# Kernel optimization log

Measured on AMD Instinct MI355X. Metric: run time of the kernel, lower is better.

Reference implementation:

```python
import jax, jax.numpy as jnp
import numpy as np

HIDDEN = 2048
N_HEADS = 32
N_KV_HEADS = 4
HEAD_DIM = 128
EPS = 1e-6
ROPE_THETA = 1000000.0
B, S = 1, 2048


def setup_inputs() -> dict:
    key = jax.random.key(0)
    ks = jax.random.split(key, 7)
    scale = 0.02
    return {
        "hidden_states": jax.random.normal(ks[0], (B, S, HIDDEN), jnp.float32),
        "wq": jax.random.normal(ks[1], (HIDDEN, N_HEADS * HEAD_DIM), jnp.float32) * scale,
        "wk": jax.random.normal(ks[2], (HIDDEN, N_KV_HEADS * HEAD_DIM), jnp.float32) * scale,
        "wv": jax.random.normal(ks[3], (HIDDEN, N_KV_HEADS * HEAD_DIM), jnp.float32) * scale,
        "wo": jax.random.normal(ks[4], (N_HEADS * HEAD_DIM, HIDDEN), jnp.float32) * scale,
        "q_norm_w": jnp.ones((HEAD_DIM,), jnp.float32),
        "k_norm_w": jnp.ones((HEAD_DIM,), jnp.float32),
    }


def _rmsnorm(x, w, eps=EPS):
    # RMSNorm over last (head_dim) axis, as in Qwen3MoeRMSNorm applied per-head
    var = jnp.mean(jnp.square(x), axis=-1, keepdims=True)
    return x * jax.lax.rsqrt(var + eps) * w


def _rope_cos_sin(seq_len, dtype):
    inv_freq = 1.0 / (ROPE_THETA ** (jnp.arange(0, HEAD_DIM, 2, dtype=jnp.float32) / HEAD_DIM))
    pos = jnp.arange(seq_len, dtype=jnp.float32)
    freqs = pos[:, None] * inv_freq[None, :]          # [S, dh/2]
    emb = jnp.concatenate([freqs, freqs], axis=-1)    # [S, dh]
    return jnp.cos(emb).astype(dtype), jnp.sin(emb).astype(dtype)


def _rotate_half(x):
    h = x.shape[-1] // 2
    return jnp.concatenate([-x[..., h:], x[..., :h]], axis=-1)


def reference(hidden_states, wq, wk, wv, wo, q_norm_w, k_norm_w):
    b, s, _ = hidden_states.shape
    # QKV projections (bias-free)
    q = (hidden_states @ wq).reshape(b, s, N_HEADS, HEAD_DIM)
    k = (hidden_states @ wk).reshape(b, s, N_KV_HEADS, HEAD_DIM)
    v = (hidden_states @ wv).reshape(b, s, N_KV_HEADS, HEAD_DIM)
    # per-head RMSNorm on Q and K
    q = _rmsnorm(q, q_norm_w)
    k = _rmsnorm(k, k_norm_w)
    # RoPE (prefill, start_pos = 0)
    cos, sin = _rope_cos_sin(s, q.dtype)              # [S, dh]
    cos = cos[None, :, None, :]
    sin = sin[None, :, None, :]
    q = q * cos + _rotate_half(q) * sin
    k = k * cos + _rotate_half(k) * sin
    # GQA: repeat KV heads to match Q heads
    groups = N_HEADS // N_KV_HEADS
    k = jnp.repeat(k, groups, axis=2)                 # [B,S,nH,dh]
    v = jnp.repeat(v, groups, axis=2)
    # causal SDPA
    scaling = HEAD_DIM ** -0.5
    scores = jnp.einsum("bqhd,bkhd->bhqk", q, k) * scaling
    causal = jnp.tril(jnp.ones((s, s), dtype=bool))
    scores = jnp.where(causal[None, None], scores, jnp.finfo(scores.dtype).min)
    probs = jax.nn.softmax(scores, axis=-1)
    attn = jnp.einsum("bhqk,bkhd->bqhd", probs, v)    # [B,S,nH,dh]
    attn = attn.reshape(b, s, N_HEADS * HEAD_DIM)
    return attn @ wo
```

## Files before the change

### kernel.cpp

```cpp
#include <hip/hip_runtime.h>
#include <stdint.h>

typedef unsigned short u16;
typedef __bf16 bf16x8 __attribute__((ext_vector_type(8)));
typedef float f32x4 __attribute__((ext_vector_type(4)));

#define SEQ 2048
#define QKV_N 5120
#define QN 4096

#if __has_builtin(__builtin_amdgcn_exp2f)
#define EXP2F __builtin_amdgcn_exp2f
#else
#define EXP2F exp2f
#endif

#define QSC (0.08838834764831845f * 1.4426950408889634f)
#define MLOG2E 17.312340490667560f

#define WAIT_VM(n) asm volatile("s_waitcnt vmcnt(" #n ")" ::: "memory")
#define WAIT_LGKM asm volatile("s_waitcnt lgkmcnt(0)" ::: "memory")
#define FENCE asm volatile("" ::: "memory")
#define BARRIER_RAW do { FENCE; __builtin_amdgcn_s_barrier(); FENCE; } while (0)

__device__ __forceinline__ u16 f2bf(float f) {
  union { float f; unsigned u; } v; v.f = f;
  unsigned r = v.u + 0x7fffu + ((v.u >> 16) & 1u);
  return (u16)(r >> 16);
}
__device__ __forceinline__ u16 f2bf_fast(float f) {
  union { float f; unsigned u; } v; v.f = f;
  return (u16)((v.u + 0x8000u) >> 16);
}
__device__ __forceinline__ float bf2f(u16 b) {
  union { unsigned u; float f; } v; v.u = ((unsigned)b) << 16;
  return v.f;
}

__device__ __forceinline__ void gl2lds16(const void* g, void* l) {
  __builtin_amdgcn_global_load_lds((const __attribute__((address_space(1))) void*)g,
                                   (__attribute__((address_space(3))) void*)l, 16, 0, 0);
}

__global__ __launch_bounds__(256) void k_prep(const float* __restrict__ hidden,
                                              const float* __restrict__ wq, const float* __restrict__ wk,
                                              const float* __restrict__ wv, const float* __restrict__ wo,
                                              u16* __restrict__ hid_bf, u16* __restrict__ WT,
                                              u16* __restrict__ woT) {
  __shared__ float t[32][33];
  int bx = blockIdx.x;
  if (bx < 4096) {
    int i = (bx * 256 + threadIdx.x) * 4;
    float4 v = *(const float4*)(hidden + i);
    ushort4 o;
    o.x = f2bf(v.x); o.y = f2bf(v.y); o.z = f2bf(v.z); o.w = f2bf(v.w);
    *(ushort4*)(hid_bf + i) = o;
    return;
  }
  const float* src; u16* dst; int R, C, cx, cy;
  if (bx < 4096 + 8192) {
    int local = bx - 4096; src = wq; dst = WT; R = 2048; C = 4096;
    cx = local & 127; cy = local >> 7;
  } else if (bx < 4096 + 8192 + 1024) {
    int local = bx - (4096 + 8192); src = wk; dst = WT + (size_t)4096 * 2048; R = 2048; C = 512;
    cx = local & 15; cy = local >> 4;
  } else if (bx < 4096 + 8192 + 2048) {
    int local = bx - (4096 + 8192 + 1024); src = wv; dst = WT + (size_t)4608 * 2048; R = 2048; C = 512;
    cx = local & 15; cy = local >> 4;
  } else {
    int local = bx - (4096 + 8192 + 2048); src = wo; dst = woT; R = 4096; C = 2048;
    cx = local & 63; cy = local >> 6;
  }
  int c0 = cx * 32, r0 = cy * 32;
  int j = threadIdx.x & 31, i0 = threadIdx.x >> 5;
#pragma unroll
  for (int p = 0; p < 4; ++p) {
    int r = i0 + p * 8;
    t[r][j] = src[(size_t)(r0 + r) * C + c0 + j];
  }
  __syncthreads();
#pragma unroll
  for (int p = 0; p < 4; ++p) {
    int r = i0 + p * 8;
    dst[(size_t)(c0 + r) * R + r0 + j] = f2bf(t[j][r]);
  }
}

__global__ __launch_bounds__(256) void k_gemm160(const u16* __restrict__ A, const u16* __restrict__ BT,
                                                 u16* __restrict__ C, int M, int N, int K) {
  __shared__ u16 As[2][128 * 64];
  __shared__ u16 Bs[2][160 * 64];
  const int tid = threadIdx.x;
  const int w = tid >> 6, lane = tid & 63, quad = lane >> 4, l15 = lane & 15;
  const int m0 = blockIdx.y * 128, n0 = blockIdx.x * 160;
  const int mw = (w & 1) * 64, nw = (w >> 1) * 80;

  f32x4 acc[4][5];
#pragma unroll
  for (int i = 0; i < 4; ++i)
#pragma unroll
    for (int j = 0; j < 5; ++j) acc[i][j] = {0.f, 0.f, 0.f, 0.f};

  auto stage = [&](int kt, int buf) {
    const int k0 = kt << 6;
#pragma unroll
    for (int p = 0; p < 4; ++p) {
      int ci = (w * 4 + p) * 64 + lane;
      int row = ci >> 3, gc = (ci & 7) ^ (row & 7);
      gl2lds16(A + (size_t)(m0 + row) * K + k0 + gc * 8, &As[buf][(w * 4 + p) * 512]);
    }
#pragma unroll
    for (int p = 0; p < 5; ++p) {
      int ci = (w * 5 + p) * 64 + lane;
      int row = ci >> 3, gc = (ci & 7) ^ (row & 7);
      gl2lds16(BT + (size_t)(n0 + row) * K + k0 + gc * 8, &Bs[buf][(w * 5 + p) * 512]);
    }
  };

  const int nk = K >> 6;
  stage(0, 0);
  for (int kt = 0; kt < nk; ++kt) {
    WAIT_LGKM;
    BARRIER_RAW;
    if (kt + 1 < nk) {
      stage(kt + 1, (kt + 1) & 1);
      WAIT_VM(9);
    } else {
      WAIT_VM(0);
    }
    BARRIER_RAW;
    const u16* Ac = As[kt & 1];
    const u16* Bc = Bs[kt & 1];
#pragma unroll
    for (int kk = 0; kk < 2; ++kk) {
      bf16x8 a[4], b[5];
#pragma unroll
      for (int mt = 0; mt < 4; ++mt) {
        int row = mw + mt * 16 + l15;
        a[mt] = *(const bf16x8*)(Ac + row * 64 + (((kk * 4 + quad) ^ (row & 7)) * 8));
      }
#pragma unroll
      for (int nt = 0; nt < 5; ++nt) {
        int row = nw + nt * 16 + l15;
        b[nt] = *(const bf16x8*)(Bc + row * 64 + (((kk * 4 + quad) ^ (row & 7)) * 8));
      }
#pragma unroll
      for (int mt = 0; mt < 4; ++mt)
#pragma unroll
        for (int nt = 0; nt < 5; ++nt)
          acc[mt][nt] = __builtin_amdgcn_mfma_f32_16x16x32_bf16(a[mt], b[nt], acc[mt][nt], 0, 0, 0);
    }
  }
#pragma unroll
  for (int mt = 0; mt < 4; ++mt)
#pragma unroll
    for (int nt = 0; nt < 5; ++nt)
#pragma unroll
      for (int r = 0; r < 4; ++r) {
        int row = m0 + mw + mt * 16 + quad * 4 + r;
        int col = n0 + nw + nt * 16 + l15;
        C[(size_t)row * N + col] = f2bf(acc[mt][nt][r]);
      }
}

__global__ __launch_bounds__(256) void k_gemm_sk(const u16* __restrict__ A, const u16* __restrict__ BT,
                                                 float* __restrict__ C, int M, int N, int K) {
  __shared__ u16 As[2][128 * 64];
  __shared__ u16 Bs[2][128 * 64];
  const int tid = threadIdx.x;
  const int w = tid >> 6, lane = tid & 63, quad = lane >> 4, l15 = lane & 15;
  const int m0 = blockIdx.y * 128, n0 = blockIdx.x * 128;
  const int mw = (w & 1) * 64, nw = (w >> 1) * 64;
  const int khalf = K >> 1;
  const int kbase = blockIdx.z * khalf;

  f32x4 acc[4][4];
#pragma unroll
  for (int i = 0; i < 4; ++i)
#pragma unroll
    for (int j = 0; j < 4; ++j) acc[i][j] = {0.f, 0.f, 0.f, 0.f};

  auto stage = [&](int kt, int buf) {
    const int k0 = kbase + (kt << 6);
#pragma unroll
    for (int p = 0; p < 4; ++p) {
      int ci = (w * 4 + p) * 64 + lane;
      int row = ci >> 3, gc = (ci & 7) ^ (row & 7);
      gl2lds16(A + (size_t)(m0 + row) * K + k0 + gc * 8, &As[buf][(w * 4 + p) * 512]);
      gl2lds16(BT + (size_t)(n0 + row) * K + k0 + gc * 8, &Bs[buf][(w * 4 + p) * 512]);
    }
  };

  const int nk = khalf >> 6;
  stage(0, 0);
  for (int kt = 0; kt < nk; ++kt) {
    WAIT_LGKM;
    BARRIER_RAW;
    if (kt + 1 < nk) {
      stage(kt + 1, (kt + 1) & 1);
      WAIT_VM(8);
    } else {
      WAIT_VM(0);
    }
    BARRIER_RAW;
    const u16* Ac = As[kt & 1];
    const u16* Bc = Bs[kt & 1];
#pragma unroll
    for (int kk = 0; kk < 2; ++kk) {
      bf16x8 a[4], b[4];
#pragma unroll
      for (int mt = 0; mt < 4; ++mt) {
        int row = mw + mt * 16 + l15;
        a[mt] = *(const bf16x8*)(Ac + row * 64 + (((kk * 4 + quad) ^ (row & 7)) * 8));
      }
#pragma unroll
      for (int nt = 0; nt < 4; ++nt) {
        int row = nw + nt * 16 + l15;
        b[nt] = *(const bf16x8*)(Bc + row * 64 + (((kk * 4 + quad) ^ (row & 7)) * 8));
      }
#pragma unroll
      for (int mt = 0; mt < 4; ++mt)
#pragma unroll
        for (int nt = 0; nt < 4; ++nt)
          acc[mt][nt] = __builtin_amdgcn_mfma_f32_16x16x32_bf16(a[mt], b[nt], acc[mt][nt], 0, 0, 0);
    }
  }
#pragma unroll
  for (int mt = 0; mt < 4; ++mt)
#pragma unroll
    for (int nt = 0; nt < 4; ++nt)
#pragma unroll
      for (int r = 0; r < 4; ++r) {
        int row = m0 + mw + mt * 16 + quad * 4 + r;
        int col = n0 + nw + nt * 16 + l15;
        atomicAdd(&C[(size_t)row * N + col], acc[mt][nt][r]);
      }
}

__global__ __launch_bounds__(256) void k_post(const u16* __restrict__ QKV,
                                              const float* __restrict__ qw, const float* __restrict__ kw,
                                              u16* __restrict__ qb, u16* __restrict__ kb,
                                              u16* __restrict__ vt) {
  __shared__ u16 t[32][34];
  int bx = blockIdx.x;
  if (bx < 2048) {
    int s = bx;
    int w = threadIdx.x >> 6, lane = threadIdx.x & 63;
    const u16* row = QKV + (size_t)s * QKV_N;
    float inv_freq = EXP2F(-(float)lane * (19.931568569324174f / 64.0f));
    float fr = (float)s * inv_freq;
    float sn, cs;
    __sincosf(fr, &sn, &cs);
    float qw0 = qw[lane], qw1 = qw[lane + 64];
    float kw0 = kw[lane], kw1 = kw[lane + 64];
    for (int item = w; item < 36; item += 4) {
      bool isq = item < 32;
      int h = isq ? item : item - 32;
      int base = isq ? h * 128 : 4096 + h * 128;
      float x0 = bf2f(row[base + lane]), x1 = bf2f(row[base + 64 + lane]);
      float ss = x0 * x0 + x1 * x1;
#pragma unroll
      for (int off = 1; off < 64; off <<= 1) ss += __shfl_xor(ss, off);
      float rr = rsqrtf(ss * (1.0f / 128.0f) + 1e-6f);
      float n0 = x0 * rr * (isq ? qw0 : kw0), n1 = x1 * rr * (isq ? qw1 : kw1);
      float y0 = n0 * cs - n1 * sn;
      float y1 = n1 * cs + n0 * sn;
      if (isq) {
        size_t o = (size_t)s * QN + h * 128 + lane;
        qb[o] = f2bf(y0 * QSC);
        qb[o + 64] = f2bf(y1 * QSC);
      } else {
        size_t o = ((size_t)h * SEQ + s) * 128 + lane;
        kb[o] = f2bf(y0);
        kb[o + 64] = f2bf(y1);
      }
    }
    return;
  }
  int local = bx - 2048;
  int s0 = (local & 63) * 32, d0 = ((local >> 6) & 3) * 32, h = local >> 8;
  int j = threadIdx.x & 31, i0 = threadIdx.x >> 5;
#pragma unroll
  for (int p = 0; p < 4; ++p) {
    int r = i0 + p * 8;
    t[r][j] = QKV[(size_t)(s0 + r) * QKV_N + 4608 + h * 128 + d0 + j];
  }
  __syncthreads();
#pragma unroll
  for (int p = 0; p < 4; ++p) {
    int r = i0 + p * 8;
    vt[((size_t)h * 128 + d0 + r) * SEQ + s0 + j] = t[j][r];
  }
}

__global__ __launch_bounds__(256, 2) void k_flash(const u16* __restrict__ qb_, const u16* __restrict__ kb,
                                                  const u16* __restrict__ vt, u16* __restrict__ attn) {
  __shared__ u16 Ks[2][64 * 128];
  __shared__ u16 Vts[2][128 * 64];
  __shared__ u16 Ps[4][2048];
  const int bx = blockIdx.x;
  const int slot = bx & 255, phase = bx >> 8;
  const int head = slot & 31;
  const int qblk = phase ? (slot >> 5) : 15 - (slot >> 5);
  const int kvh = head >> 3;
  const int q0 = qblk * 128;
  const int tid = threadIdx.x, w = tid >> 6, lane = tid & 63, quad = lane >> 4, l15 = lane & 15;
  const int rowlo0 = q0 + w * 32, rowlo1 = rowlo0 + 16;

  bf16x8 qf[2][4];
#pragma unroll
  for (int mt = 0; mt < 2; ++mt) {
    const u16* qrow = qb_ + (size_t)(rowlo0 + mt * 16 + l15) * QN + head * 128;
#pragma unroll
    for (int ks = 0; ks < 4; ++ks) qf[mt][ks] = *(const bf16x8*)(qrow + ks * 32 + quad * 8);
  }
  f32x4 o[2][8];
#pragma unroll
  for (int mt = 0; mt < 2; ++mt)
#pragma unroll
    for (int i = 0; i < 8; ++i) o[mt][i] = {0.f, 0.f, 0.f, 0.f};
  float lr[2][4] = {{0.f, 0.f, 0.f, 0.f}, {0.f, 0.f, 0.f, 0.f}};

  const u16* kbase = kb + (size_t)kvh * SEQ * 128;
  const u16* vbase = vt + (size_t)kvh * 128 * SEQ;
  u16* pw = Ps[w];

  auto stage = [&](int ti, int buf) {
    const int t0 = ti * 64;
#pragma unroll
    for (int p = 0; p < 4; ++p) {
      int ci = (w * 4 + p) * 64 + lane;
      {
        int row = ci >> 4, gc = (ci & 15) ^ (row & 15);
        gl2lds16(kbase + (size_t)(t0 + row) * 128 + gc * 8, &Ks[buf][(w * 4 + p) * 512]);
      }
      {
        int d = ci >> 3, gc = (ci & 7) ^ (d & 7);
        gl2lds16(vbase + (size_t)d * SEQ + t0 + gc * 8, &Vts[buf][(w * 4 + p) * 512]);
      }
    }
  };

  const int nT = 2 * qblk + 2;
  stage(0, 0);
  for (int ti = 0; ti < nT; ++ti) {
    const int t0 = ti * 64;
    WAIT_LGKM;
    BARRIER_RAW;
    if (ti + 1 < nT) {
      stage(ti + 1, (ti + 1) & 1);
      WAIT_VM(8);
    } else {
      WAIT_VM(0);
    }
    BARRIER_RAW;
    const u16* Kc = Ks[ti & 1];
    const u16* Vc = Vts[ti & 1];

    const bool a0 = t0 < rowlo0 + 16;
    const bool a1 = t0 < rowlo1 + 16;
    if (a1) {
      f32x4 sa[2][4];
#pragma unroll
      for (int mt = 0; mt < 2; ++mt)
#pragma unroll
        for (int nt = 0; nt < 4; ++nt) sa[mt][nt] = {0.f, 0.f, 0.f, 0.f};
#pragma unroll
      for (int nt = 0; nt < 4; ++nt) {
        int row = nt * 16 + l15;
#pragma unroll
        for (int ks = 0; ks < 4; ++ks) {
          bf16x8 kf = *(const bf16x8*)(Kc + row * 128 + (((ks * 4 + quad) ^ (row & 15)) * 8));
          if (a0) sa[0][nt] = __builtin_amdgcn_mfma_f32_16x16x32_bf16(qf[0][ks], kf, sa[0][nt], 0, 0, 0);
          sa[1][nt] = __builtin_amdgcn_mfma_f32_16x16x32_bf16(qf[1][ks], kf, sa[1][nt], 0, 0, 0);
        }
      }
#pragma unroll
      for (int mt = 0; mt < 2; ++mt) {
        if (mt == 0 && !a0) continue;
        const int rl = rowlo0 + mt * 16;
        const bool domask = (t0 + 63 > rl);
        u16* pm = pw + mt * 1024;
#pragma unroll
        for (int nt = 0; nt < 4; ++nt)
#pragma unroll
          for (int r = 0; r < 4; ++r) {
            float p = EXP2F(sa[mt][nt][r] - MLOG2E);
            if (domask) {
              int tcol = t0 + nt * 16 + l15;
              int qrow = rl + quad * 4 + r;
              p = (tcol > qrow) ? 0.f : p;
            }
            sa[mt][nt][r] = p;
            pm[(quad * 4 + r) * 64 + ((nt ^ quad) << 4) + l15] = f2bf_fast(p);
          }
#pragma unroll
        for (int r = 0; r < 4; ++r)
          lr[mt][r] += sa[mt][0][r] + sa[mt][1][r] + sa[mt][2][r] + sa[mt][3][r];
      }
      WAIT_LGKM;
#pragma unroll
      for (int ks2 = 0; ks2 < 2; ++ks2) {
        int col = (ks2 * 32 + quad * 8) ^ ((l15 >> 2) << 4);
        bf16x8 pa0, pa1;
        if (a0) pa0 = *(const bf16x8*)(pw + l15 * 64 + col);
        pa1 = *(const bf16x8*)(pw + 1024 + l15 * 64 + col);
#pragma unroll
        for (int nt2 = 0; nt2 < 8; ++nt2) {
          int d = nt2 * 16 + l15;
          bf16x8 vf = *(const bf16x8*)(Vc + d * 64 + (((ks2 * 4 + quad) ^ (d & 7)) * 8));
          if (a0) o[0][nt2] = __builtin_amdgcn_mfma_f32_16x16x32_bf16(pa0, vf, o[0][nt2], 0, 0, 0);
          o[1][nt2] = __builtin_amdgcn_mfma_f32_16x16x32_bf16(pa1, vf, o[1][nt2], 0, 0, 0);
        }
      }
    }
  }
#pragma unroll
  for (int mt = 0; mt < 2; ++mt) {
    float inv[4];
#pragma unroll
    for (int r = 0; r < 4; ++r) {
      float s = lr[mt][r];
      s += __shfl_xor(s, 1);
      s += __shfl_xor(s, 2);
      s += __shfl_xor(s, 4);
      s += __shfl_xor(s, 8);
      inv[r] = 1.0f / s;
    }
#pragma unroll
    for (int nt2 = 0; nt2 < 8; ++nt2)
#pragma unroll
      for (int r = 0; r < 4; ++r) {
        size_t idx = (size_t)(rowlo0 + mt * 16 + quad * 4 + r) * QN + head * 128 + nt2 * 16 + l15;
        attn[idx] = f2bf_fast(o[mt][nt2][r] * inv[r]);
      }
  }
}

extern "C" void kernel_launch(void* const* d_in, const int* in_sizes, int n_in,
                              void* d_out, int out_size, void* d_ws, size_t ws_size,
                              hipStream_t stream) {
  const float* hidden = (const float*)d_in[0];
  const float* wq = (const float*)d_in[1];
  const float* wk = (const float*)d_in[2];
  const float* wv = (const float*)d_in[3];
  const float* wo = (const float*)d_in[4];
  const float* qnw = (const float*)d_in[5];
  const float* knw = (const float*)d_in[6];
  float* out = (float*)d_out;

  char* ws = (char*)d_ws;
  u16* hid_bf = (u16*)(ws);
  u16* WT = (u16*)(ws + 8388608);
  u16* woT = (u16*)(ws + 29360128);
  u16* QKV = (u16*)(ws + 46137344);
  u16* q_bf = (u16*)(ws + 88080384);
  u16* k_bf = (u16*)(ws + 104857600);
  u16* vt = (u16*)(ws + 106954752);
  u16* attn = (u16*)(ws + 109051904);

  hipMemsetAsync(d_out, 0, (size_t)2048 * 2048 * 4, stream);
  k_prep<<<22528, 256, 0, stream>>>(hidden, wq, wk, wv, wo, hid_bf, WT, woT);
  k_gemm160<<<dim3(32, 16), 256, 0, stream>>>(hid_bf, WT, QKV, 2048, 5120, 2048);
  k_post<<<3072, 256, 0, stream>>>(QKV, qnw, knw, q_bf, k_bf, vt);
  k_flash<<<512, 256, 0, stream>>>(q_bf, k_bf, vt, attn);
  k_gemm_sk<<<dim3(16, 16, 2), 256, 0, stream>>>(attn, woT, out, 2048, 2048, 4096);
}
```

Before: 317.5 us.

## Enlarge flash-attention query tile to 256 rows with paired causal work items

The flash kernel now gives each block 256 query rows (four 16-row M-tiles per wave, interleaved across waves) instead of 128, so each staged K/V tile feeds twice as many MFMAs. Each block processes two causal items (qi and 7-qi) in sequence to balance work, and the grid drops to 256 blocks with launch bounds of 1 block per CU. The P scratch buffer switches from an XOR swizzle to a padded 72-element stride. The larger register footprint and lower occupancy may hurt latency hiding, and 256 blocks may not fill all CUs.

```diff
diff --git a/kernel.cpp b/kernel.cpp
--- a/kernel.cpp
+++ b/kernel.cpp
@@ -293,33 +293,15 @@
   }
 }
 
-__global__ __launch_bounds__(256, 2) void k_flash(const u16* __restrict__ qb_, const u16* __restrict__ kb,
+__global__ __launch_bounds__(256, 1) void k_flash(const u16* __restrict__ qb_, const u16* __restrict__ kb,
                                                   const u16* __restrict__ vt, u16* __restrict__ attn) {
   __shared__ u16 Ks[2][64 * 128];
   __shared__ u16 Vts[2][128 * 64];
-  __shared__ u16 Ps[4][2048];
+  __shared__ u16 Ps[4][64 * 72];
   const int bx = blockIdx.x;
-  const int slot = bx & 255, phase = bx >> 8;
-  const int head = slot & 31;
-  const int qblk = phase ? (slot >> 5) : 15 - (slot >> 5);
+  const int head = bx & 31, qi = bx >> 5;
   const int kvh = head >> 3;
-  const int q0 = qblk * 128;
   const int tid = threadIdx.x, w = tid >> 6, lane = tid & 63, quad = lane >> 4, l15 = lane & 15;
-  const int rowlo0 = q0 + w * 32, rowlo1 = rowlo0 + 16;
-
-  bf16x8 qf[2][4];
-#pragma unroll
-  for (int mt = 0; mt < 2; ++mt) {
-    const u16* qrow = qb_ + (size_t)(rowlo0 + mt * 16 + l15) * QN + head * 128;
-#pragma unroll
-    for (int ks = 0; ks < 4; ++ks) qf[mt][ks] = *(const bf16x8*)(qrow + ks * 32 + quad * 8);
-  }
-  f32x4 o[2][8];
-#pragma unroll
-  for (int mt = 0; mt < 2; ++mt)
-#pragma unroll
-    for (int i = 0; i < 8; ++i) o[mt][i] = {0.f, 0.f, 0.f, 0.f};
-  float lr[2][4] = {{0.f, 0.f, 0.f, 0.f}, {0.f, 0.f, 0.f, 0.f}};
 
   const u16* kbase = kb + (size_t)kvh * SEQ * 128;
   const u16* vbase = vt + (size_t)kvh * 128 * SEQ;
@@ -341,28 +323,56 @@
     }
   };
 
-  const int nT = 2 * qblk + 2;
-  stage(0, 0);
-  for (int ti = 0; ti < nT; ++ti) {
-    const int t0 = ti * 64;
+#pragma unroll 1
+  for (int item = 0; item < 2; ++item) {
+    const int qblk = item ? (7 - qi) : qi;
+    const int q0 = qblk * 256;
+
+    bf16x8 qf[4][4];
+#pragma unroll
+    for (int mt = 0; mt < 4; ++mt) {
+      const u16* qrow = qb_ + (size_t)(q0 + mt * 64 + w * 16 + l15) * QN + head * 128;
+#pragma unroll
+      for (int ks = 0; ks < 4; ++ks) qf[mt][ks] = *(const bf16x8*)(qrow + ks * 32 + quad * 8);
+    }
+    f32x4 o[4][8];
+#pragma unroll
+    for (int mt = 0; mt < 4; ++mt)
+#pragma unroll
+      for (int i = 0; i < 8; ++i) o[mt][i] = {0.f, 0.f, 0.f, 0.f};
+    float lr[4][4];
+#pragma unroll
+    for (int mt = 0; mt < 4; ++mt)
+#pragma unroll
+      for (int r = 0; r < 4; ++r) lr[mt][r] = 0.f;
+
+    const int nT = 4 * qblk + 4;
     WAIT_LGKM;
     BARRIER_RAW;
-    if (ti + 1 < nT) {
-      stage(ti + 1, (ti + 1) & 1);
-      WAIT_VM(8);
-    } else {
-      WAIT_VM(0);
-    }
-    BARRIER_RAW;
-    const u16* Kc = Ks[ti & 1];
-    const u16* Vc = Vts[ti & 1];
-
-    const bool a0 = t0 < rowlo0 + 16;
-    const bool a1 = t0 < rowlo1 + 16;
-    if (a1) {
-      f32x4 sa[2][4];
-#pragma unroll
-      for (int mt = 0; mt < 2; ++mt)
+    stage(0, 0);
+#pragma unroll 1
+    for (int ti = 0; ti < nT; ++ti) {
+      const int t0 = ti * 64;
+      WAIT_LGKM;
+      BARRIER_RAW;
+      if (ti + 1 < nT) {
+        stage(ti + 1, (ti + 1) & 1);
+        WAIT_VM(8);
+      } else {
+        WAIT_VM(0);
+      }
+      BARRIER_RAW;
+      const u16* Kc = Ks[ti & 1];
+      const u16* Vc = Vts[ti & 1];
+
+      bool am[4];
+#pragma unroll
+      for (int mt = 0; mt < 4; ++mt) am[mt] = t0 < q0 + mt * 64 + w * 16 + 16;
+      if (!am[3]) continue;
+
+      f32x4 sa[4][4];
+#pragma unroll
+      for (int mt = 0; mt < 4; ++mt)
 #pragma unroll
         for (int nt = 0; nt < 4; ++nt) sa[mt][nt] = {0.f, 0.f, 0.f, 0.f};
 #pragma unroll
@@ -371,16 +381,17 @@
 #pragma unroll
         for (int ks = 0; ks < 4; ++ks) {
           bf16x8 kf = *(const bf16x8*)(Kc + row * 128 + (((ks * 4 + quad) ^ (row & 15)) * 8));
-          if (a0) sa[0][nt] = __builtin_amdgcn_mfma_f32_16x16x32_bf16(qf[0][ks], kf, sa[0][nt], 0, 0, 0);
-          sa[1][nt] = __builtin_amdgcn_mfma_f32_16x16x32_bf16(qf[1][ks], kf, sa[1][nt], 0, 0, 0);
+#pragma unroll
+          for (int mt = 0; mt < 4; ++mt)
+            if (am[mt]) sa[mt][nt] = __builtin_amdgcn_mfma_f32_16x16x32_bf16(qf[mt][ks], kf, sa[mt][nt], 0, 0, 0);
         }
       }
 #pragma unroll
-      for (int mt = 0; mt < 2; ++mt) {
-        if (mt == 0 && !a0) continue;
-        const int rl = rowlo0 + mt * 16;
+      for (int mt = 0; mt < 4; ++mt) {
+        if (!am[mt]) continue;
+        const int rl = q0 + mt * 64 + w * 16;
         const bool domask = (t0 + 63 > rl);
-        u16* pm = pw + mt * 1024;
+        u16* pm = pw + mt * 16 * 72;
 #pragma unroll
         for (int nt = 0; nt < 4; ++nt)
 #pragma unroll
@@ -392,7 +403,7 @@
               p = (tcol > qrow) ? 0.f : p;
             }
             sa[mt][nt][r] = p;
-            pm[(quad * 4 + r) * 64 + ((nt ^ quad) << 4) + l15] = f2bf_fast(p);
+            pm[(quad * 4 + r) * 72 + nt * 16 + l15] = f2bf_fast(p);
           }
 #pragma unroll
         for (int r = 0; r < 4; ++r)
@@ -401,39 +412,40 @@
       WAIT_LGKM;
 #pragma unroll
       for (int ks2 = 0; ks2 < 2; ++ks2) {
-        int col = (ks2 * 32 + quad * 8) ^ ((l15 >> 2) << 4);
-        bf16x8 pa0, pa1;
-        if (a0) pa0 = *(const bf16x8*)(pw + l15 * 64 + col);
-        pa1 = *(const bf16x8*)(pw + 1024 + l15 * 64 + col);
+        bf16x8 pa[4];
+#pragma unroll
+        for (int mt = 0; mt < 4; ++mt)
+          if (am[mt]) pa[mt] = *(const bf16x8*)(pw + (mt * 16 + l15) * 72 + ks2 * 32 + quad * 8);
 #pragma unroll
         for (int nt2 = 0; nt2 < 8; ++nt2) {
           int d = nt2 * 16 + l15;
           bf16x8 vf = *(const bf16x8*)(Vc + d * 64 + (((ks2 * 4 + quad) ^ (d & 7)) * 8));
-          if (a0) o[0][nt2] = __builtin_amdgcn_mfma_f32_16x16x32_bf16(pa0, vf, o[0][nt2], 0, 0, 0);
-          o[1][nt2] = __builtin_amdgcn_mfma_f32_16x16x32_bf16(pa1, vf, o[1][nt2], 0, 0, 0);
+#pragma unroll
+          for (int mt = 0; mt < 4; ++mt)
+            if (am[mt]) o[mt][nt2] = __builtin_amdgcn_mfma_f32_16x16x32_bf16(pa[mt], vf, o[mt][nt2], 0, 0, 0);
         }
       }
     }
-  }
-#pragma unroll
-  for (int mt = 0; mt < 2; ++mt) {
-    float inv[4];
-#pragma unroll
-    for (int r = 0; r < 4; ++r) {
-      float s = lr[mt][r];
-      s += __shfl_xor(s, 1);
-      s += __shfl_xor(s, 2);
-      s += __shfl_xor(s, 4);
-      s += __shfl_xor(s, 8);
-      inv[r] = 1.0f / s;
-    }
-#pragma unroll
-    for (int nt2 = 0; nt2 < 8; ++nt2)
+#pragma unroll
+    for (int mt = 0; mt < 4; ++mt) {
+      float inv[4];
 #pragma unroll
       for (int r = 0; r < 4; ++r) {
-        size_t idx = (size_t)(rowlo0 + mt * 16 + quad * 4 + r) * QN + head * 128 + nt2 * 16 + l15;
-        attn[idx] = f2bf_fast(o[mt][nt2][r] * inv[r]);
-      }
+        float s = lr[mt][r];
+        s += __shfl_xor(s, 1);
+        s += __shfl_xor(s, 2);
+        s += __shfl_xor(s, 4);
+        s += __shfl_xor(s, 8);
+        inv[r] = 1.0f / s;
+      }
+#pragma unroll
+      for (int nt2 = 0; nt2 < 8; ++nt2)
+#pragma unroll
+        for (int r = 0; r < 4; ++r) {
+          size_t idx = (size_t)(q0 + mt * 64 + w * 16 + quad * 4 + r) * QN + head * 128 + nt2 * 16 + l15;
+          attn[idx] = f2bf_fast(o[mt][nt2][r] * inv[r]);
+        }
+    }
   }
 }
 
@@ -463,6 +475,6 @@
   k_prep<<<22528, 256, 0, stream>>>(hidden, wq, wk, wv, wo, hid_bf, WT, woT);
   k_gemm160<<<dim3(32, 16), 256, 0, stream>>>(hid_bf, WT, QKV, 2048, 5120, 2048);
   k_post<<<3072, 256, 0, stream>>>(QKV, qnw, knw, q_bf, k_bf, vt);
-  k_flash<<<512, 256, 0, stream>>>(q_bf, k_bf, vt, attn);
+  k_flash<<<256, 256, 0, stream>>>(q_bf, k_bf, vt, attn);
   k_gemm_sk<<<dim3(16, 16, 2), 256, 0, stream>>>(attn, woT, out, 2048, 2048, 4096);
 }
```

Result: slower. 420.2 us (+32.3%).

## Replace double-buffered K/V staging with single buffer and split K/V waits

Applied to the files above, without the earlier changes.

Removes the double-buffered K/V LDS prefetch and instead loads K and V for the current tile each iteration into a single buffer. It waits only for the K loads before the QK^T MFMAs and waits for V just before the PV MFMAs, so V loading overlaps with the score/softmax compute. This halves K/V LDS usage, which may allow more resident blocks, and drops the min-blocks launch bound. In exchange it loses cross-iteration prefetch, so K load latency is exposed each tile, and an extra barrier is added per iteration.

```diff
diff --git a/kernel.cpp b/kernel.cpp
--- a/kernel.cpp
+++ b/kernel.cpp
@@ -293,10 +293,10 @@
   }
 }
 
-__global__ __launch_bounds__(256, 2) void k_flash(const u16* __restrict__ qb_, const u16* __restrict__ kb,
-                                                  const u16* __restrict__ vt, u16* __restrict__ attn) {
-  __shared__ u16 Ks[2][64 * 128];
-  __shared__ u16 Vts[2][128 * 64];
+__global__ __launch_bounds__(256) void k_flash(const u16* __restrict__ qb_, const u16* __restrict__ kb,
+                                               const u16* __restrict__ vt, u16* __restrict__ attn) {
+  __shared__ u16 Ks[64 * 128];
+  __shared__ u16 Vts[128 * 64];
   __shared__ u16 Ps[4][2048];
   const int bx = blockIdx.x;
   const int slot = bx & 255, phase = bx >> 8;
@@ -325,37 +325,24 @@
   const u16* vbase = vt + (size_t)kvh * 128 * SEQ;
   u16* pw = Ps[w];
 
-  auto stage = [&](int ti, int buf) {
+  const int nT = 2 * qblk + 2;
+  for (int ti = 0; ti < nT; ++ti) {
     const int t0 = ti * 64;
+    BARRIER_RAW;
 #pragma unroll
     for (int p = 0; p < 4; ++p) {
       int ci = (w * 4 + p) * 64 + lane;
-      {
-        int row = ci >> 4, gc = (ci & 15) ^ (row & 15);
-        gl2lds16(kbase + (size_t)(t0 + row) * 128 + gc * 8, &Ks[buf][(w * 4 + p) * 512]);
-      }
-      {
-        int d = ci >> 3, gc = (ci & 7) ^ (d & 7);
-        gl2lds16(vbase + (size_t)d * SEQ + t0 + gc * 8, &Vts[buf][(w * 4 + p) * 512]);
-      }
-    }
-  };
-
-  const int nT = 2 * qblk + 2;
-  stage(0, 0);
-  for (int ti = 0; ti < nT; ++ti) {
-    const int t0 = ti * 64;
-    WAIT_LGKM;
-    BARRIER_RAW;
-    if (ti + 1 < nT) {
-      stage(ti + 1, (ti + 1) & 1);
-      WAIT_VM(8);
-    } else {
-      WAIT_VM(0);
-    }
-    BARRIER_RAW;
-    const u16* Kc = Ks[ti & 1];
-    const u16* Vc = Vts[ti & 1];
+      int row = ci >> 4, gc = (ci & 15) ^ (row & 15);
+      gl2lds16(kbase + (size_t)(t0 + row) * 128 + gc * 8, Ks + (w * 4 + p) * 512);
+    }
+#pragma unroll
+    for (int p = 0; p < 4; ++p) {
+      int ci = (w * 4 + p) * 64 + lane;
+      int d = ci >> 3, gc = (ci & 7) ^ (d & 7);
+      gl2lds16(vbase + (size_t)d * SEQ + t0 + gc * 8, Vts + (w * 4 + p) * 512);
+    }
+    WAIT_VM(4);
+    BARRIER_RAW;
 
     const bool a0 = t0 < rowlo0 + 16;
     const bool a1 = t0 < rowlo1 + 16;
@@ -370,7 +357,7 @@
         int row = nt * 16 + l15;
 #pragma unroll
         for (int ks = 0; ks < 4; ++ks) {
-          bf16x8 kf = *(const bf16x8*)(Kc + row * 128 + (((ks * 4 + quad) ^ (row & 15)) * 8));
+          bf16x8 kf = *(const bf16x8*)(Ks + row * 128 + (((ks * 4 + quad) ^ (row & 15)) * 8));
           if (a0) sa[0][nt] = __builtin_amdgcn_mfma_f32_16x16x32_bf16(qf[0][ks], kf, sa[0][nt], 0, 0, 0);
           sa[1][nt] = __builtin_amdgcn_mfma_f32_16x16x32_bf16(qf[1][ks], kf, sa[1][nt], 0, 0, 0);
         }
@@ -398,7 +385,11 @@
         for (int r = 0; r < 4; ++r)
           lr[mt][r] += sa[mt][0][r] + sa[mt][1][r] + sa[mt][2][r] + sa[mt][3][r];
       }
-      WAIT_LGKM;
+    }
+    WAIT_VM(0);
+    WAIT_LGKM;
+    BARRIER_RAW;
+    if (a1) {
 #pragma unroll
       for (int ks2 = 0; ks2 < 2; ++ks2) {
         int col = (ks2 * 32 + quad * 8) ^ ((l15 >> 2) << 4);
@@ -408,7 +399,7 @@
 #pragma unroll
         for (int nt2 = 0; nt2 < 8; ++nt2) {
           int d = nt2 * 16 + l15;
-          bf16x8 vf = *(const bf16x8*)(Vc + d * 64 + (((ks2 * 4 + quad) ^ (d & 7)) * 8));
+          bf16x8 vf = *(const bf16x8*)(Vts + d * 64 + (((ks2 * 4 + quad) ^ (d & 7)) * 8));
           if (a0) o[0][nt2] = __builtin_amdgcn_mfma_f32_16x16x32_bf16(pa0, vf, o[0][nt2], 0, 0, 0);
           o[1][nt2] = __builtin_amdgcn_mfma_f32_16x16x32_bf16(pa1, vf, o[1][nt2], 0, 0, 0);
         }
```

New measurement: 319.8 us. About the same (+0.7%).
